# Optimization experiments

Measured on AMD Instinct MI355X. Metric: run time of the kernel, lower is better.

The kernel has to match this reference:

```python
import jax, jax.numpy as jnp
import numpy as np

T, B, D, H, Q = 512, 256, 128, 128, 8


def _qgate(z, theta):
    """Analytic simulation of the QGate circuit.

    Circuit: start |0..0>, RX(z_j) then trainable RX(theta_j) on each wire j
    (RX(a)RX(b)=RX(a+b)), then a CNOT ring w->(w+1)%Q, then <Z_w> on each wire.
    RX(phi)|0> gives <Z>=cos(phi) and independent wires; the CNOT ring permutes
    computational basis states so bit_w = XOR_{j<=w} a_j for w>=1 and
    bit_0 = XOR_{j>=1} a_j, hence <Z_w> = prod_{j<=w} cos(phi_j) for w>=1 and
    <Z_0> = prod_{j>=1} cos(phi_j). Exact, no 2^Q statevector needed.
    """
    c = jnp.cos(z + theta)                      # (B, Q)
    cp = jnp.cumprod(c, axis=-1)                # (B, Q)
    z0 = jnp.prod(c[:, 1:], axis=-1, keepdims=True)
    return jnp.concatenate([z0, cp[:, 1:]], axis=-1)


def setup_inputs() -> dict:
    key = jax.random.key(0)
    ks = jax.random.split(key, 25)
    inp = {"inputs": jax.random.normal(ks[0], (T, B, D), dtype=jnp.float32)}
    s_in = 1.0 / np.sqrt(D + H)
    s_q = 1.0 / np.sqrt(Q)
    names = ["f", "i", "g", "o"]
    for n, gname in enumerate(names):
        k = ks[1 + 6 * n: 1 + 6 * (n + 1)]
        inp["W" + gname] = jax.random.uniform(k[0], (Q, D + H), jnp.float32, -s_in, s_in)
        inp["b" + gname] = jax.random.uniform(k[1], (Q,), jnp.float32, -s_in, s_in)
        inp["th" + gname] = jax.random.normal(k[2], (Q,), jnp.float32)  # trainable RX angles
        inp["U" + gname] = jax.random.uniform(k[3], (H, Q), jnp.float32, -s_q, s_q)
        inp["c" + gname] = jax.random.uniform(k[4], (H,), jnp.float32, -s_q, s_q)
    return inp


def reference(inputs, Wf, bf, thf, Uf, cf,
              Wi, bi, thi, Ui, ci,
              Wg, bg, thg, Ug, cg,
              Wo, bo, tho, Uo, co):
    bsz = inputs.shape[1]
    hdim = Uf.shape[0]
    h0 = jnp.zeros((bsz, hdim), inputs.dtype)
    c0 = jnp.zeros((bsz, hdim), inputs.dtype)

    def gate(comb, W, b, th, U, cb):
        return _qgate(comb @ W.T + b, th) @ U.T + cb

    def step(carry, x):
        hx, cx = carry
        comb = jnp.concatenate([x, hx], axis=1)          # (B, D+H)
        f = jax.nn.sigmoid(gate(comb, Wf, bf, thf, Uf, cf))
        i = jax.nn.sigmoid(gate(comb, Wi, bi, thi, Ui, ci))
        g = jnp.tanh(gate(comb, Wg, bg, thg, Ug, cg))
        o = jax.nn.sigmoid(gate(comb, Wo, bo, tho, Uo, co))
        cx = f * cx + i * g
        hx = o * jnp.tanh(cx)
        return (hx, cx), hx

    (hx, cx), outs = jax.lax.scan(step, (h0, c0), inputs)
    return outs, hx, cx
```

## Files before the change

### kernel.cpp

```cpp
#include <hip/hip_runtime.h>

#define TT 512
#define BB 256
#define DD 128
#define HH 128
#define QQ 8

struct Params {
    const float* x;
    const float* W[4];
    const float* b[4];
    const float* th[4];
    const float* U[4];
    const float* cb[4];
    float* out;
};

__device__ __forceinline__ float sigm_fast(float x) {
    return __builtin_amdgcn_rcpf(1.f + __expf(-x));
}
__device__ __forceinline__ float tanh_fast(float x) {
    return 1.f - 2.f * __builtin_amdgcn_rcpf(__expf(2.f * x) + 1.f);
}
template<int CTRL>
__device__ __forceinline__ float dpp_mov(float x) {
    int r = __builtin_amdgcn_update_dpp(0, __float_as_int(x), CTRL, 0xF, 0xF, true);
    return __int_as_float(r);
}
__device__ __forceinline__ void bar_lds() {
    asm volatile("s_waitcnt lgkmcnt(0)\n\ts_barrier" ::: "memory");
}

__global__ __launch_bounds__(256, 1) void qlstm(Params p) {
    __shared__ __align__(16) float xbuf[2][8][144];
    __shared__ __align__(16) float hbuf[144];
    __shared__ float pre[512];

    const int tid = threadIdx.x;
    const int bId = blockIdx.x;
    const int ln  = tid & 63;
    const int wv  = tid >> 6;
    const int qub = (tid >> 3) & 7;
    const int part = tid & 7;

    float Wreg[32];
    {
        const float* Wg = p.W[wv] + qub * (DD + HH) + part * 32;
        #pragma unroll
        for (int j = 0; j < 32; ++j) Wreg[j] = Wg[j];
    }
    const float breg  = p.b[wv][qub] + p.th[wv][qub];

    float Ua[8], Ub[8];
    #pragma unroll
    for (int j = 0; j < 8; ++j) {
        Ua[j] = p.U[wv][ln * QQ + j];
        Ub[j] = p.U[wv][(ln + 64) * QQ + j];
    }
    const float cba = p.cb[wv][ln];
    const float cbb = p.cb[wv][ln + 64];

    float cst = 0.f;
    float hn_last = 0.f;

    if (tid < 128) hbuf[tid + 4 * (tid >> 5)] = 0.f;

    const int xc_col  = (ln & 31) * 4;
    const int xc_half = ln >> 5;
    const int xc_slot = xc_col + 4 * (xc_col >> 5);
    float4 xr[4];
    #pragma unroll
    for (int j = 0; j < 4; ++j) xr[j] = make_float4(0.f, 0.f, 0.f, 0.f);

    if (wv == 3) {
        #pragma unroll
        for (int j = 0; j < 4; ++j) {
            const int row = 2 * j + xc_half;
            float4 v = *(const float4*)(p.x + ((size_t)row * BB + bId) * DD + xc_col);
            *(float4*)&xbuf[0][row][xc_slot] = v;
        }
        #pragma unroll
        for (int j = 0; j < 4; ++j) {
            const int row = 8 + 2 * j + xc_half;
            xr[j] = *(const float4*)(p.x + ((size_t)row * BB + bId) * DD + xc_col);
        }
    }
    __syncthreads();

    for (int t = 0; t < TT; ++t) {
        if (((t & 7) == 0) && wv == 3) {
            const int tch = (t >> 3) + 1;
            if (tch < TT / 8) {
                #pragma unroll
                for (int j = 0; j < 4; ++j) {
                    const int row = tch * 8 + 2 * j + xc_half;
                    xr[j] = *(const float4*)(p.x + ((size_t)row * BB + bId) * DD + xc_col);
                }
            }
        }

        const float* src = (part < 4) ? &xbuf[(t >> 3) & 1][t & 7][36 * part]
                                      : &hbuf[36 * (part - 4)];
        float a0 = 0.f, a1 = 0.f, a2 = 0.f, a3 = 0.f;
        #pragma unroll
        for (int j4 = 0; j4 < 8; ++j4) {
            float4 c4 = *(const float4*)(src + 4 * j4);
            a0 = fmaf(Wreg[4*j4+0], c4.x, a0);
            a1 = fmaf(Wreg[4*j4+1], c4.y, a1);
            a2 = fmaf(Wreg[4*j4+2], c4.z, a2);
            a3 = fmaf(Wreg[4*j4+3], c4.w, a3);
        }
        float acc = (a0 + a1) + (a2 + a3);

        acc += dpp_mov<0xB1>(acc);
        acc += dpp_mov<0x4E>(acc);
        acc += dpp_mov<0x141>(acc);

        const float cv = __cosf(acc + breg);
        float c[8];
        #pragma unroll
        for (int j = 0; j < 8; ++j) {
            c[j] = __int_as_float(
                __builtin_amdgcn_ds_bpermute(j * 32, __float_as_int(cv)));
        }
        const float q1 = c[0] * c[1];
        const float q2 = q1 * c[2];
        const float q3 = q2 * c[3];
        const float q4 = q3 * c[4];
        const float q5 = q4 * c[5];
        const float q6 = q5 * c[6];
        const float q7 = q6 * c[7];
        float q0 = c[1] * c[2];
        q0 *= c[3]; q0 *= c[4]; q0 *= c[5]; q0 *= c[6]; q0 *= c[7];

        float pa = fmaf(Ua[0], q0, cba); float pb = fmaf(Ub[0], q0, cbb);
        pa = fmaf(Ua[1], q1, pa);        pb = fmaf(Ub[1], q1, pb);
        pa = fmaf(Ua[2], q2, pa);        pb = fmaf(Ub[2], q2, pb);
        pa = fmaf(Ua[3], q3, pa);        pb = fmaf(Ub[3], q3, pb);
        pa = fmaf(Ua[4], q4, pa);        pb = fmaf(Ub[4], q4, pb);
        pa = fmaf(Ua[5], q5, pa);        pb = fmaf(Ub[5], q5, pb);
        pa = fmaf(Ua[6], q6, pa);        pb = fmaf(Ub[6], q6, pb);
        pa = fmaf(Ua[7], q7, pa);        pb = fmaf(Ub[7], q7, pb);
        pre[wv * 128 + ln]      = pa;
        pre[wv * 128 + 64 + ln] = pb;

        bar_lds();

        if (tid < 128) {
            float fg = sigm_fast(pre[tid]);
            float ig = sigm_fast(pre[128 + tid]);
            float gg = tanh_fast(pre[256 + tid]);
            float og = sigm_fast(pre[384 + tid]);
            cst = fmaf(fg, cst, ig * gg);
            float hn = og * tanh_fast(cst);
            hn_last = hn;
            hbuf[tid + 4 * (tid >> 5)] = hn;
            p.out[(size_t)(t * BB + bId) * HH + tid] = hn;
        } else if (wv == 3 && (t & 7) == 7) {
            const int tch = (t >> 3) + 1;
            if (tch < TT / 8) {
                #pragma unroll
                for (int j = 0; j < 4; ++j) {
                    const int row = 2 * j + xc_half;
                    *(float4*)&xbuf[tch & 1][row][xc_slot] = xr[j];
                }
            }
        }
        bar_lds();
    }

    if (tid < 128) {
        p.out[(size_t)TT * BB * HH + (size_t)bId * HH + tid] = hn_last;
        p.out[(size_t)TT * BB * HH + (size_t)BB * HH + (size_t)bId * HH + tid] = cst;
    }
}

extern "C" void kernel_launch(void* const* d_in, const int* in_sizes, int n_in,
                              void* d_out, int out_size, void* d_ws, size_t ws_size,
                              hipStream_t stream) {
    (void)in_sizes; (void)n_in; (void)out_size; (void)d_ws; (void)ws_size;
    Params p;
    p.x = (const float*)d_in[0];
    for (int g = 0; g < 4; ++g) {
        p.W[g]  = (const float*)d_in[1 + 5 * g + 0];
        p.b[g]  = (const float*)d_in[1 + 5 * g + 1];
        p.th[g] = (const float*)d_in[1 + 5 * g + 2];
        p.U[g]  = (const float*)d_in[1 + 5 * g + 3];
        p.cb[g] = (const float*)d_in[1 + 5 * g + 4];
    }
    p.out = (float*)d_out;
    hipLaunchKernelGGL(qlstm, dim3(BB), dim3(256), 0, stream, p);
}
```

Measured before the change: 407.4 us.

## Precompute x-projection one step ahead on idle waves and use DPP scans for qgate products

Splits each gate's input projection so that waves 2-3, which are otherwise idle during the cell update, compute the x·W part for the next timestep into a double-buffered LDS slot. This shortens the serial critical path to only the h·W dot product. The qubit cumulative products now use DPP row-broadcast multiplies plus readlane instead of eight ds_bpermute calls. The exp scaling constants are folded into U and cb so the activations can use exp2 directly, and waves 0-1 read their own preactivation from registers. The cost is more register pressure from the extra Wx array, added LDS traffic, and a changed timing for the x-buffer refill that must stay correctly ordered.

```diff
diff --git a/kernel.cpp b/kernel.cpp
--- a/kernel.cpp
+++ b/kernel.cpp
@@ -16,17 +16,22 @@
     float* out;
 };
 
-__device__ __forceinline__ float sigm_fast(float x) {
-    return __builtin_amdgcn_rcpf(1.f + __expf(-x));
-}
-__device__ __forceinline__ float tanh_fast(float x) {
-    return 1.f - 2.f * __builtin_amdgcn_rcpf(__expf(2.f * x) + 1.f);
-}
+__device__ __forceinline__ float rcp_f(float x)  { return __builtin_amdgcn_rcpf(x); }
+__device__ __forceinline__ float exp2_f(float x) { return __builtin_amdgcn_exp2f(x); }
+
 template<int CTRL>
 __device__ __forceinline__ float dpp_mov(float x) {
     int r = __builtin_amdgcn_update_dpp(0, __float_as_int(x), CTRL, 0xF, 0xF, true);
     return __int_as_float(r);
 }
+template<int CTRL, int RM>
+__device__ __forceinline__ float dpp_mul1(float x) {
+    int r = __builtin_amdgcn_update_dpp(0x3f800000 , __float_as_int(x),
+                                        CTRL, RM, 0xF, false);
+    return __int_as_float(r);
+}
+#define RDLANE(v, l) __int_as_float(__builtin_amdgcn_readlane(__float_as_int(v), (l)))
+
 __device__ __forceinline__ void bar_lds() {
     asm volatile("s_waitcnt lgkmcnt(0)\n\ts_barrier" ::: "memory");
 }
@@ -35,30 +40,42 @@
     __shared__ __align__(16) float xbuf[2][8][144];
     __shared__ __align__(16) float hbuf[144];
     __shared__ float pre[512];
+    __shared__ float zxbuf[2][32];
 
     const int tid = threadIdx.x;
     const int bId = blockIdx.x;
     const int ln  = tid & 63;
     const int wv  = tid >> 6;
-    const int qub = (tid >> 3) & 7;
-    const int part = tid & 7;
-
-    float Wreg[32];
+    const int qub = ln >> 3;
+    const int part8 = ln & 7;
+
+    float Wh[16];
     {
-        const float* Wg = p.W[wv] + qub * (DD + HH) + part * 32;
-        #pragma unroll
-        for (int j = 0; j < 32; ++j) Wreg[j] = Wg[j];
-    }
-    const float breg  = p.b[wv][qub] + p.th[wv][qub];
-
+        const float* Wg = p.W[wv] + qub * (DD + HH) + DD + part8 * 16;
+        #pragma unroll
+        for (int j = 0; j < 16; ++j) Wh[j] = Wg[j];
+    }
+    const float breg = p.b[wv][qub] + p.th[wv][qub];
+
+    const int gz = 2 * (wv - 2) + (ln >> 5);
+    const int qz = (ln >> 2) & 7;
+    const int pz = ln & 3;
+    float Wx[32];
+    if (wv >= 2) {
+        const float* Wg = p.W[gz] + qz * (DD + HH) + pz * 32;
+        #pragma unroll
+        for (int j = 0; j < 32; ++j) Wx[j] = Wg[j];
+    }
+
+    const float esc = (wv == 2) ? 2.885390081777927f : -1.442695040888963f;
     float Ua[8], Ub[8];
     #pragma unroll
     for (int j = 0; j < 8; ++j) {
-        Ua[j] = p.U[wv][ln * QQ + j];
-        Ub[j] = p.U[wv][(ln + 64) * QQ + j];
-    }
-    const float cba = p.cb[wv][ln];
-    const float cbb = p.cb[wv][ln + 64];
+        Ua[j] = p.U[wv][ln * QQ + j] * esc;
+        Ub[j] = p.U[wv][(ln + 64) * QQ + j] * esc;
+    }
+    const float cba = p.cb[wv][ln] * esc;
+    const float cbb = p.cb[wv][ln + 64] * esc;
 
     float cst = 0.f;
     float hn_last = 0.f;
@@ -79,14 +96,28 @@
             float4 v = *(const float4*)(p.x + ((size_t)row * BB + bId) * DD + xc_col);
             *(float4*)&xbuf[0][row][xc_slot] = v;
         }
-        #pragma unroll
-        for (int j = 0; j < 4; ++j) {
-            const int row = 8 + 2 * j + xc_half;
-            xr[j] = *(const float4*)(p.x + ((size_t)row * BB + bId) * DD + xc_col);
-        }
     }
     __syncthreads();
 
+    if (wv >= 2) {
+        const float* xrow = &xbuf[0][0][36 * pz];
+        float b0 = 0.f, b1 = 0.f, b2 = 0.f, b3 = 0.f;
+        #pragma unroll
+        for (int i = 0; i < 8; ++i) {
+            float4 c4 = *(const float4*)(xrow + 4 * i);
+            b0 = fmaf(Wx[4*i+0], c4.x, b0);
+            b1 = fmaf(Wx[4*i+1], c4.y, b1);
+            b2 = fmaf(Wx[4*i+2], c4.z, b2);
+            b3 = fmaf(Wx[4*i+3], c4.w, b3);
+        }
+        float zx2 = (b0 + b1) + (b2 + b3);
+        zx2 += dpp_mov<0xB1>(zx2);
+        zx2 += dpp_mov<0x4E>(zx2);
+        if ((ln & 3) == 0) zxbuf[0][8 * gz + qz] = zx2;
+    }
+    __syncthreads();
+
+    #pragma unroll 8
     for (int t = 0; t < TT; ++t) {
         if (((t & 7) == 0) && wv == 3) {
             const int tch = (t >> 3) + 1;
@@ -99,39 +130,40 @@
             }
         }
 
-        const float* src = (part < 4) ? &xbuf[(t >> 3) & 1][t & 7][36 * part]
-                                      : &hbuf[36 * (part - 4)];
+        const float zxs = zxbuf[t & 1][8 * wv + qub];
+        const float* hsrc = &hbuf[16 * part8 + 4 * (part8 >> 1)];
         float a0 = 0.f, a1 = 0.f, a2 = 0.f, a3 = 0.f;
         #pragma unroll
-        for (int j4 = 0; j4 < 8; ++j4) {
-            float4 c4 = *(const float4*)(src + 4 * j4);
-            a0 = fmaf(Wreg[4*j4+0], c4.x, a0);
-            a1 = fmaf(Wreg[4*j4+1], c4.y, a1);
-            a2 = fmaf(Wreg[4*j4+2], c4.z, a2);
-            a3 = fmaf(Wreg[4*j4+3], c4.w, a3);
+        for (int i = 0; i < 4; ++i) {
+            float4 c4 = *(const float4*)(hsrc + 4 * i);
+            a0 = fmaf(Wh[4*i+0], c4.x, a0);
+            a1 = fmaf(Wh[4*i+1], c4.y, a1);
+            a2 = fmaf(Wh[4*i+2], c4.z, a2);
+            a3 = fmaf(Wh[4*i+3], c4.w, a3);
         }
         float acc = (a0 + a1) + (a2 + a3);
-
         acc += dpp_mov<0xB1>(acc);
         acc += dpp_mov<0x4E>(acc);
         acc += dpp_mov<0x141>(acc);
-
-        const float cv = __cosf(acc + breg);
-        float c[8];
-        #pragma unroll
-        for (int j = 0; j < 8; ++j) {
-            c[j] = __int_as_float(
-                __builtin_amdgcn_ds_bpermute(j * 32, __float_as_int(cv)));
-        }
-        const float q1 = c[0] * c[1];
-        const float q2 = q1 * c[2];
-        const float q3 = q2 * c[3];
-        const float q4 = q3 * c[4];
-        const float q5 = q4 * c[5];
-        const float q6 = q5 * c[6];
-        const float q7 = q6 * c[7];
-        float q0 = c[1] * c[2];
-        q0 *= c[3]; q0 *= c[4]; q0 *= c[5]; q0 *= c[6]; q0 *= c[7];
+        acc += zxs + breg;
+
+        const float cv = __cosf(acc);
+        float v = cv;
+        v *= dpp_mul1<0x118, 0xF>(v);
+        v *= dpp_mul1<0x142, 0xA>(v);
+        v *= dpp_mul1<0x143, 0xC>(v);
+        float u = (ln < 8) ? 1.f : cv;
+        u *= dpp_mul1<0x118, 0xF>(u);
+        u *= dpp_mul1<0x142, 0xA>(u);
+        u *= dpp_mul1<0x143, 0xC>(u);
+        const float q0 = RDLANE(u, 63);
+        const float q1 = RDLANE(v, 8);
+        const float q2 = RDLANE(v, 16);
+        const float q3 = RDLANE(v, 24);
+        const float q4 = RDLANE(v, 32);
+        const float q5 = RDLANE(v, 40);
+        const float q6 = RDLANE(v, 48);
+        const float q7 = RDLANE(v, 56);
 
         float pa = fmaf(Ua[0], q0, cba); float pb = fmaf(Ub[0], q0, cbb);
         pa = fmaf(Ua[1], q1, pa);        pb = fmaf(Ub[1], q1, pb);
@@ -147,23 +179,47 @@
         bar_lds();
 
         if (tid < 128) {
-            float fg = sigm_fast(pre[tid]);
-            float ig = sigm_fast(pre[128 + tid]);
-            float gg = tanh_fast(pre[256 + tid]);
-            float og = sigm_fast(pre[384 + tid]);
+            float p_f = (wv == 0) ? pa : pre[tid];
+            float p_i = (wv == 1) ? pb : pre[128 + tid];
+            float p_g = pre[256 + tid];
+            float p_o = pre[384 + tid];
+            float fg = rcp_f(1.f + exp2_f(p_f));
+            float ig = rcp_f(1.f + exp2_f(p_i));
+            float gg = 1.f - 2.f * rcp_f(1.f + exp2_f(p_g));
+            float og = rcp_f(1.f + exp2_f(p_o));
             cst = fmaf(fg, cst, ig * gg);
-            float hn = og * tanh_fast(cst);
+            float tc = 1.f - 2.f * rcp_f(1.f + exp2_f(cst * 2.885390081777927f));
+            float hn = og * tc;
             hn_last = hn;
             hbuf[tid + 4 * (tid >> 5)] = hn;
             p.out[(size_t)(t * BB + bId) * HH + tid] = hn;
-        } else if (wv == 3 && (t & 7) == 7) {
-            const int tch = (t >> 3) + 1;
-            if (tch < TT / 8) {
+        } else {
+            if (wv == 3 && (t & 7) == 6) {
+                const int tch = (t >> 3) + 1;
+                if (tch < TT / 8) {
+                    #pragma unroll
+                    for (int j = 0; j < 4; ++j) {
+                        const int row = 2 * j + xc_half;
+                        *(float4*)&xbuf[tch & 1][row][xc_slot] = xr[j];
+                    }
+                }
+            }
+            if (t < TT - 1) {
+                const int tn = t + 1;
+                const float* xrow = &xbuf[(tn >> 3) & 1][tn & 7][36 * pz];
+                float b0 = 0.f, b1 = 0.f, b2 = 0.f, b3 = 0.f;
                 #pragma unroll
-                for (int j = 0; j < 4; ++j) {
-                    const int row = 2 * j + xc_half;
-                    *(float4*)&xbuf[tch & 1][row][xc_slot] = xr[j];
+                for (int i = 0; i < 8; ++i) {
+                    float4 c4 = *(const float4*)(xrow + 4 * i);
+                    b0 = fmaf(Wx[4*i+0], c4.x, b0);
+                    b1 = fmaf(Wx[4*i+1], c4.y, b1);
+                    b2 = fmaf(Wx[4*i+2], c4.z, b2);
+                    b3 = fmaf(Wx[4*i+3], c4.w, b3);
                 }
+                float zx2 = (b0 + b1) + (b2 + b3);
+                zx2 += dpp_mov<0xB1>(zx2);
+                zx2 += dpp_mov<0x4E>(zx2);
+                if ((ln & 3) == 0) zxbuf[tn & 1][8 * gz + qz] = zx2;
             }
         }
         bar_lds();
```

After: 371.0 us. 1.1x faster.
